# Kernel tuning notes

Hardware: AMD Instinct MI355X
Metric: run time of the kernel (lower is better)

The kernel has to match this reference:

```python
import jax, jax.numpy as jnp
import numpy as np

N, E, IN_DIM, H, D, EDGE_DIM, T = 50000, 800000, 128, 4, 32, 32, 8
NEG_SLOPE = 0.2


def setup_inputs() -> dict:
    key = jax.random.key(0)
    ks = jax.random.split(key, 12)
    s = 0.1  # xavier-ish scale
    return {
        "h": jax.random.normal(ks[0], (N, IN_DIM), jnp.float32),
        "W": jax.random.normal(ks[1], (IN_DIM, D * H), jnp.float32) * s,
        "edge_emb": jax.random.normal(ks[2], (T, EDGE_DIM), jnp.float32) * s,
        "W_r": jax.random.normal(ks[3], (T, EDGE_DIM, EDGE_DIM * H), jnp.float32) * s,
        "a_l": jax.random.normal(ks[4], (1, H, D), jnp.float32) * s,
        "a_r": jax.random.normal(ks[5], (1, H, D), jnp.float32) * s,
        "a_e": jax.random.normal(ks[6], (1, H, EDGE_DIM), jnp.float32) * s,
        "res_w": jax.random.normal(ks[7], (IN_DIM, D * H), jnp.float32) * s,
        "res_b": jnp.zeros((D * H,), jnp.float32),
        "row": jax.random.randint(ks[8], (E,), 0, N),  # src node per edge
        "col": jax.random.randint(ks[9], (E,), 0, N),  # dst node per edge
        "etype": jax.random.randint(ks[10], (E,), 0, T),
    }


def reference(h, W, edge_emb, W_r, a_l, a_r, a_e, res_w, res_b, row, col, etype):
    # node projection: [N, H, D]
    emb = (h @ W).reshape(-1, H, D)

    # TypedLinear on edge-type embeddings. Since edge features depend only on
    # etype, compute the per-type result once, then gather per edge.
    e_t = jnp.einsum('te,tef->tf', edge_emb, W_r).reshape(T, H, EDGE_DIM)
    h_e_t = (a_e * e_t).sum(-1)            # [T, H]

    h_l = (a_l * emb).sum(-1)              # [N, H]
    h_r = (a_r * emb).sum(-1)              # [N, H]
    scores = h_l[row] + h_r[col] + h_e_t[etype]          # [E, H]
    scores = jax.nn.leaky_relu(scores, NEG_SLOPE)

    # segment softmax over edges sharing the same destination node (col)
    m = jax.ops.segment_max(scores, col, num_segments=N)  # [N, H]
    ex = jnp.exp(scores - m[col])
    denom = jax.ops.segment_sum(ex, col, num_segments=N)
    alpha = ex / denom[col]                # [E, H]

    # u_mul_e + scatter-sum to destination nodes
    msg = emb[row] * alpha[:, :, None]     # [E, H, D]
    agg = jax.ops.segment_sum(msg, col, num_segments=N)   # [N, H, D]

    # original permutes to [N, D, H] before flattening (d-major layout)
    out = jnp.transpose(agg, (0, 2, 1)).reshape(-1, D * H)
    out = out + h @ res_w + res_b          # residual
    return jax.nn.elu(out)
```

## Files before the change

kernel.cpp:

```cpp
#include <hip/hip_runtime.h>
#include <math.h>

#define NH 4
#define EDIM 32
#define NEG_SLOPE 0.2f
#define BSH 5
#define CHK 32

typedef __attribute__((ext_vector_type(8))) short short8;
typedef __attribute__((ext_vector_type(4))) float f32x4;
typedef __attribute__((ext_vector_type(2))) float f32x2;

__device__ __forceinline__ unsigned short f2bf(float f) {
    unsigned int x = __builtin_bit_cast(unsigned int, f);
    unsigned int r = (x + 0x7fffu + ((x >> 16) & 1u)) >> 16;
    return (unsigned short)r;
}
__device__ __forceinline__ float bf2f(unsigned short u) {
    unsigned int x = ((unsigned int)u) << 16;
    return __builtin_bit_cast(float, x);
}

__global__ __launch_bounds__(256) void k_prep(
    const float* __restrict__ W, const float* __restrict__ Rw,
    unsigned short* __restrict__ Wt, unsigned short* __restrict__ Rwt,
    const float* __restrict__ edge_emb, const float* __restrict__ W_r,
    const float* __restrict__ a_e, float* __restrict__ h_e_t)
{
    int tid = threadIdx.x;
    if (blockIdx.x < 64) {
        int idx = blockIdx.x * 256 + tid;
        int n = idx >> 7, k = idx & 127;
        Wt[n * 128 + k]  = f2bf(W[k * 128 + n]);
        Rwt[n * 128 + k] = f2bf(Rw[k * 128 + n]);
        return;
    }
    int t = blockIdx.x - 64;
    if (tid < 128) {
        int rem = tid;
        float v = 0.f;
#pragma unroll
        for (int e = 0; e < EDIM; ++e)
            v += edge_emb[t * EDIM + e] * W_r[(size_t)(t * EDIM + e) * 128 + rem];
        v *= a_e[rem];
#pragma unroll
        for (int off = 16; off >= 1; off >>= 1)
            v += __shfl_xor(v, off);
        if ((rem & 31) == 0) h_e_t[t * NH + (rem >> 5)] = v;
    }
}

__global__ __launch_bounds__(256) void k_gemm_fill(
    const float* __restrict__ A, const unsigned short* __restrict__ Wt,
    const unsigned short* __restrict__ Rwt, const float* __restrict__ Rb,
    const float* __restrict__ a_l, const float* __restrict__ a_r,
    unsigned short* __restrict__ EmbBf, unsigned short* __restrict__ ResBf,
    float* __restrict__ h_l, float* __restrict__ h_r, int M,
    const int* __restrict__ row, const int* __restrict__ col,
    const int* __restrict__ etype, int* __restrict__ cnt,
    unsigned* __restrict__ ebuf, int E, int NB, int nFill)
{
    __shared__ char lds[32768];
    int tid = threadIdx.x;

    if ((int)blockIdx.x < nFill) {
        int* bins = (int*)lds;
        for (int i = tid; i < NB; i += 256) bins[i] = 0;
        __syncthreads();
        int fb = blockIdx.x;
        int lo = fb * 8192;
#pragma unroll 8
        for (int u = 0; u < 32; ++u) {
            int i = lo + tid + u * 256;
            if (i < E) {
                int c = col[i];
                int bk = c >> BSH;
                int slot = atomicAdd(&bins[bk], 1);
                if (slot < CHK)
                    ebuf[((size_t)bk * nFill + fb) * CHK + slot] =
                        (unsigned)row[i] | ((unsigned)etype[i] << 16)
                      | ((unsigned)(c & 31) << 24);
            }
        }
        __syncthreads();
        for (int i = tid; i < NB; i += 256) {
            int c = bins[i]; if (c > CHK) c = CHK;
            cnt[i * nFill + fb] = c;
        }
        return;
    }

    int m0 = ((int)blockIdx.x - nFill) * 64;
#pragma unroll
    for (int i = 0; i < 4; ++i) {
        int c = tid + 256 * i;
        int r = c >> 4, kc = c & 15;
        int grow = m0 + r;
        float4 v0 = make_float4(0.f, 0.f, 0.f, 0.f), v1 = v0;
        if (grow < M) {
            v0 = *(const float4*)&A[(size_t)grow * 128 + kc * 8];
            v1 = *(const float4*)&A[(size_t)grow * 128 + kc * 8 + 4];
        }
        union { unsigned short u[8]; uint4 v; } p;
        p.u[0] = f2bf(v0.x); p.u[1] = f2bf(v0.y); p.u[2] = f2bf(v0.z); p.u[3] = f2bf(v0.w);
        p.u[4] = f2bf(v1.x); p.u[5] = f2bf(v1.y); p.u[6] = f2bf(v1.z); p.u[7] = f2bf(v1.w);
        int b = (r * 256 + kc * 16) ^ ((r & 7) << 4);
        *(uint4*)&lds[b] = p.v;
    }

    int w = tid >> 6, lane = tid & 63;
    int g = lane >> 4, l15 = lane & 15;
    int lrow = w * 16 + l15;

    auto stageB = [&](const unsigned short* src) {
#pragma unroll
        for (int i = 0; i < 4; ++i) {
            int c = tid + 256 * i;
            int n2 = c >> 4, kc = c & 15;
            uint4 v = *(const uint4*)&src[n2 * 128 + kc * 8];
            int b = 16384 + ((n2 * 256 + kc * 16) ^ ((n2 & 7) << 4));
            *(uint4*)&lds[b] = v;
        }
    };
    auto computeHalf = [&](f32x4* accp, const short8* a) {
#pragma unroll
        for (int f = 0; f < 4; ++f) {
            int n2 = f * 16 + l15;
            int nsw = (n2 & 7) << 4;
#pragma unroll
            for (int s = 0; s < 4; ++s) {
                short8 b = *(const short8*)&lds[16384 + ((n2 * 256 + s * 64 + g * 16) ^ nsw)];
                accp[f] = __builtin_amdgcn_mfma_f32_16x16x32_bf16(a[s], b, accp[f], 0, 0, 0);
            }
        }
    };

    stageB(Wt);
    __syncthreads();

    short8 a[4];
#pragma unroll
    for (int s = 0; s < 4; ++s)
        a[s] = *(const short8*)&lds[(lrow * 256 + s * 64 + g * 16) ^ ((lrow & 7) << 4)];

    f32x4 acc[8];
#pragma unroll
    for (int f = 0; f < 8; ++f) acc[f] = (f32x4){0.f, 0.f, 0.f, 0.f};

    computeHalf(&acc[0], a);
    __syncthreads();
    stageB(Wt + 64 * 128);
    __syncthreads();
    computeHalf(&acc[4], a);

#pragma unroll
    for (int f = 0; f < 8; ++f) {
        int col2 = f * 16 + l15;
#pragma unroll
        for (int reg = 0; reg < 4; ++reg) {
            int grow = m0 + w * 16 + g * 4 + reg;
            if (grow < M) EmbBf[(size_t)grow * 128 + col2] = f2bf(acc[f][reg]);
        }
    }
    {
        float alv[8], arv[8];
#pragma unroll
        for (int f = 0; f < 8; ++f) {
            alv[f] = a_l[f * 16 + l15];
            arv[f] = a_r[f * 16 + l15];
        }
#pragma unroll
        for (int reg = 0; reg < 4; ++reg) {
            float4 hl4, hr4;
#pragma unroll
            for (int hh = 0; hh < 4; ++hh) {
                float pl = alv[2 * hh] * acc[2 * hh][reg] + alv[2 * hh + 1] * acc[2 * hh + 1][reg];
                float pr = arv[2 * hh] * acc[2 * hh][reg] + arv[2 * hh + 1] * acc[2 * hh + 1][reg];
#pragma unroll
                for (int off = 8; off >= 1; off >>= 1) {
                    pl += __shfl_xor(pl, off);
                    pr += __shfl_xor(pr, off);
                }
                (&hl4.x)[hh] = pl;
                (&hr4.x)[hh] = pr;
            }
            int grow = m0 + w * 16 + g * 4 + reg;
            if (l15 == 0 && grow < M) {
                *(float4*)&h_l[(size_t)grow * 4] = hl4;
                *(float4*)&h_r[(size_t)grow * 4] = hr4;
            }
        }
    }

    __syncthreads();
    stageB(Rwt);
    __syncthreads();
#pragma unroll
    for (int f = 0; f < 8; ++f) acc[f] = (f32x4){0.f, 0.f, 0.f, 0.f};
    computeHalf(&acc[0], a);
    __syncthreads();
    stageB(Rwt + 64 * 128);
    __syncthreads();
    computeHalf(&acc[4], a);

#pragma unroll
    for (int f = 0; f < 8; ++f) {
        int col2 = f * 16 + l15;
        float bias = Rb[col2];
#pragma unroll
        for (int reg = 0; reg < 4; ++reg) {
            int grow = m0 + w * 16 + g * 4 + reg;
            if (grow < M) ResBf[(size_t)grow * 128 + col2] = f2bf(acc[f][reg] + bias);
        }
    }
}

__global__ __launch_bounds__(512) void k_sort_aggregate(
    const unsigned* __restrict__ ebuf, const int* __restrict__ cnt, int nF,
    const float* __restrict__ h_l, const float* __restrict__ h_e_t,
    const float* __restrict__ h_r, const unsigned short* __restrict__ embBf,
    const unsigned short* __restrict__ resBf, float* __restrict__ out, int N)
{
    __shared__ int stage[1024];
    __shared__ int sedge[1024];
    __shared__ int chcnt[128];
    __shared__ int choff[132];
    __shared__ int cnt32[32];
    __shared__ int scn32[33];
    __shared__ char shalpha[8 * 1536];

    int b = blockIdx.x;
    int tid = threadIdx.x;
    int w = tid >> 6, lane = tid & 63;

    if (tid < 32) cnt32[tid] = 0;
    if (tid < 64) {
        int i0 = tid * 2, i1 = i0 + 1;
        int c0 = (i0 < nF) ? cnt[(size_t)b * nF + i0] : 0;
        int c1 = (i1 < nF) ? cnt[(size_t)b * nF + i1] : 0;
        chcnt[i0] = c0; chcnt[i1] = c1;
        int s = c0 + c1;
#pragma unroll
        for (int off = 1; off < 64; off <<= 1) {
            int u2 = __shfl_up(s, off);
            if (tid >= off) s += u2;
        }
        choff[i0] = s - c1 - c0;
        choff[i1] = s - c1;
        if (tid == 63) choff[128] = s;
    }
    __syncthreads();
    int m = choff[128];

#pragma unroll
    for (int itc = 0; itc < 2; ++itc) {
        int ch = itc * 64 + (tid >> 3);
        int sl = tid & 7;
        int c = chcnt[ch];
        if (sl < c) {
            int v = (int)ebuf[((size_t)b * nF + ch) * CHK + sl];
            stage[choff[ch] + sl] = v;
            atomicAdd(&cnt32[(v >> 24) & 31], 1);
        }
    }
    for (int ch = w; ch < 128; ch += 8) {
        int c = chcnt[ch];
        if (c > 8 && lane < c - 8) {
            int v = (int)ebuf[((size_t)b * nF + ch) * CHK + 8 + lane];
            stage[choff[ch] + 8 + lane] = v;
            atomicAdd(&cnt32[(v >> 24) & 31], 1);
        }
    }
    __syncthreads();

    if (tid < 32) {
        int v = cnt32[tid];
        int s = v;
#pragma unroll
        for (int off = 1; off < 32; off <<= 1) {
            int u2 = __shfl_up(s, off);
            if (tid >= off) s += u2;
        }
        scn32[tid + 1] = s;
        if (tid == 0) scn32[0] = 0;
        cnt32[tid] = s - v;
    }
    __syncthreads();
    for (int i = tid; i < m; i += 512) {
        int e = stage[i];
        int p = atomicAdd(&cnt32[(e >> 24) & 31], 1);
        sedge[p] = e & 0x00FFFFFF;
    }
    __syncthreads();

    int myh = lane >> 4;
    int l31 = lane & 31;
    int sel = lane >> 5;
    int hq = l31 >> 3;
    int loff = l31 * 8;
    char* wb = &shalpha[w * 1536];
    const char* ab2 = wb + 256 + hq * 260;
    const char* embByte = (const char*)embBf;

    for (int it = 0; it < 4; ++it) {
        int nd = it * 8 + w;
        int n = b * 32 + nd;
        if (n >= N) break;
        int st0 = scn32[nd];
        int deg = scn32[nd + 1] - st0;
        float4 hrv = *(const float4*)&h_r[(size_t)n * 4];

        if (deg <= 64) {
            bool act = lane < deg;
            float p0 = 0.f, p1 = 0.f, p2 = 0.f, p3 = 0.f;
            int roval = 0;
            if (act) {
                int pk = sedge[st0 + lane];
                roval = (pk & 0xffff) << 8;
                float4 hl = *(const float4*)&h_l[(size_t)(pk & 0xffff) * 4];
                float4 he = *(const float4*)&h_e_t[(size_t)(pk >> 16) * 4];
                float sc0 = hl.x + he.x + hrv.x; sc0 = sc0 > 0.f ? sc0 : NEG_SLOPE * sc0;
                float sc1 = hl.y + he.y + hrv.y; sc1 = sc1 > 0.f ? sc1 : NEG_SLOPE * sc1;
                float sc2 = hl.z + he.z + hrv.z; sc2 = sc2 > 0.f ? sc2 : NEG_SLOPE * sc2;
                float sc3 = hl.w + he.w + hrv.w; sc3 = sc3 > 0.f ? sc3 : NEG_SLOPE * sc3;
                p0 = __expf(sc0); p1 = __expf(sc1);
                p2 = __expf(sc2); p3 = __expf(sc3);
            }
            *(int*)(wb + lane * 4) = roval;
            *(float*)(wb + 256 + 0 * 260 + lane * 4) = p0;
            *(float*)(wb + 256 + 1 * 260 + lane * 4) = p1;
            *(float*)(wb + 256 + 2 * 260 + lane * 4) = p2;
            *(float*)(wb + 256 + 3 * 260 + lane * 4) = p3;

            float d0 = p0, d1 = p1, d2 = p2, d3 = p3;
#pragma unroll
            for (int off = 32; off >= 1; off >>= 1) {
                d0 += __shfl_xor(d0, off); d1 += __shfl_xor(d1, off);
                d2 += __shfl_xor(d2, off); d3 += __shfl_xor(d3, off);
            }
            float den = hq == 0 ? d0 : hq == 1 ? d1 : hq == 2 ? d2 : d3;
            float inv = (deg > 0) ? __builtin_amdgcn_rcpf(den) : 0.f;

            f32x4 acc4 = (f32x4){0.f, 0.f, 0.f, 0.f};
            for (int q = 0; q < deg; q += 8) {
                int ro[4]; float aq[4];
#pragma unroll
                for (int u = 0; u < 4; ++u) {
                    int qe = q + 2 * u + sel;
                    ro[u] = *(const int*)(wb + qe * 4);
                    aq[u] = *(const float*)(ab2 + qe * 4);
                }
                uint2 ev[4];
#pragma unroll
                for (int u = 0; u < 4; ++u)
                    ev[u] = *(const uint2*)(embByte + (size_t)(unsigned)(ro[u] + loff));
#pragma unroll
                for (int u = 0; u < 4; ++u) {
                    f32x4 ef;
                    ef.x = __builtin_bit_cast(float, ev[u].x << 16);
                    ef.y = __builtin_bit_cast(float, ev[u].x & 0xffff0000u);
                    ef.z = __builtin_bit_cast(float, ev[u].y << 16);
                    ef.w = __builtin_bit_cast(float, ev[u].y & 0xffff0000u);
                    acc4 = __builtin_elementwise_fma(
                        ef, (f32x4){aq[u], aq[u], aq[u], aq[u]}, acc4);
                }
            }
            acc4.x += __shfl_xor(acc4.x, 32);
            acc4.y += __shfl_xor(acc4.y, 32);
            acc4.z += __shfl_xor(acc4.z, 32);
            acc4.w += __shfl_xor(acc4.w, 32);
            float vlo = sel ? acc4.z : acc4.x;
            float vhi = sel ? acc4.w : acc4.y;

            int j0 = l31 * 4 + sel * 2;
            int h0 = j0 >> 5, dd = j0 & 31;
            size_t ob = (size_t)n * 128;
            float o0 = vlo * inv + bf2f(resBf[ob + dd * 4 + h0]);
            float o1 = vhi * inv + bf2f(resBf[ob + (dd + 1) * 4 + h0]);
            out[ob + dd * 4 + h0] = o0 > 0.f ? o0 : expm1f(o0);
            out[ob + (dd + 1) * 4 + h0] = o1 > 0.f ? o1 : expm1f(o1);
        } else {
            f32x2 acc2 = (f32x2){0.f, 0.f};
            float d0 = 0.f, d1 = 0.f, d2 = 0.f, d3 = 0.f;
            for (int base2 = 0; base2 < deg; base2 += 64) {
                int el = base2 + lane;
                if (el < deg) {
                    int pk = sedge[st0 + el];
                    float4 hl = *(const float4*)&h_l[(size_t)(pk & 0xffff) * 4];
                    float4 he = *(const float4*)&h_e_t[(size_t)(pk >> 16) * 4];
                    float sc0 = hl.x + he.x + hrv.x; sc0 = sc0 > 0.f ? sc0 : NEG_SLOPE * sc0;
                    float sc1 = hl.y + he.y + hrv.y; sc1 = sc1 > 0.f ? sc1 : NEG_SLOPE * sc1;
                    float sc2 = hl.z + he.z + hrv.z; sc2 = sc2 > 0.f ? sc2 : NEG_SLOPE * sc2;
                    float sc3 = hl.w + he.w + hrv.w; sc3 = sc3 > 0.f ? sc3 : NEG_SLOPE * sc3;
                    d0 += __expf(sc0); d1 += __expf(sc1);
                    d2 += __expf(sc2); d3 += __expf(sc3);
                }
            }
#pragma unroll
            for (int off = 32; off >= 1; off >>= 1) {
                d0 += __shfl_xor(d0, off); d1 += __shfl_xor(d1, off);
                d2 += __shfl_xor(d2, off); d3 += __shfl_xor(d3, off);
            }
            float den = myh == 0 ? d0 : myh == 1 ? d1 : myh == 2 ? d2 : d3;
            float inv = __builtin_amdgcn_rcpf(den);
            for (int base2 = 0; base2 < deg; base2 += 64) {
                int el = base2 + lane;
                float p0 = 0.f, p1 = 0.f, p2 = 0.f, p3 = 0.f;
                int r = 0;
                if (el < deg) {
                    int pk = sedge[st0 + el];
                    r = pk & 0xffff;
                    float4 hl = *(const float4*)&h_l[(size_t)r * 4];
                    float4 he = *(const float4*)&h_e_t[(size_t)(pk >> 16) * 4];
                    float sc0 = hl.x + he.x + hrv.x; sc0 = sc0 > 0.f ? sc0 : NEG_SLOPE * sc0;
                    float sc1 = hl.y + he.y + hrv.y; sc1 = sc1 > 0.f ? sc1 : NEG_SLOPE * sc1;
                    float sc2 = hl.z + he.z + hrv.z; sc2 = sc2 > 0.f ? sc2 : NEG_SLOPE * sc2;
                    float sc3 = hl.w + he.w + hrv.w; sc3 = sc3 > 0.f ? sc3 : NEG_SLOPE * sc3;
                    p0 = __expf(sc0); p1 = __expf(sc1);
                    p2 = __expf(sc2); p3 = __expf(sc3);
                }
                int cmax = (deg - base2 < 64) ? (deg - base2) : 64;
                for (int qq = 0; qq < cmax; ++qq) {
                    int rq = __shfl(r, qq);
                    float a0 = __shfl(p0, qq), a1 = __shfl(p1, qq);
                    float a2 = __shfl(p2, qq), a3 = __shfl(p3, qq);
                    float aqv = myh == 0 ? a0 : myh == 1 ? a1 : myh == 2 ? a2 : a3;
                    unsigned int ev = *(const unsigned int*)&embBf[(size_t)rq * 128 + lane * 2];
                    f32x2 ef;
                    ef.x = __builtin_bit_cast(float, ev << 16);
                    ef.y = __builtin_bit_cast(float, ev & 0xffff0000u);
                    acc2 = __builtin_elementwise_fma(ef, (f32x2){aqv, aqv}, acc2);
                }
            }
            int j0 = lane * 2;
            int h0 = j0 >> 5, dd0 = j0 & 31;
            size_t ob = (size_t)n * 128;
            float o0 = acc2.x * inv + bf2f(resBf[ob + dd0 * 4 + h0]);
            float o1 = acc2.y * inv + bf2f(resBf[ob + (dd0 + 1) * 4 + h0]);
            out[ob + dd0 * 4 + h0] = o0 > 0.f ? o0 : expm1f(o0);
            out[ob + (dd0 + 1) * 4 + h0] = o1 > 0.f ? o1 : expm1f(o1);
        }
    }
}

extern "C" void kernel_launch(void* const* d_in, const int* in_sizes, int n_in,
                              void* d_out, int out_size, void* d_ws, size_t ws_size,
                              hipStream_t stream)
{
    const float* h        = (const float*)d_in[0];
    const float* W        = (const float*)d_in[1];
    const float* edge_emb = (const float*)d_in[2];
    const float* W_r      = (const float*)d_in[3];
    const float* a_l      = (const float*)d_in[4];
    const float* a_r      = (const float*)d_in[5];
    const float* a_e      = (const float*)d_in[6];
    const float* res_w    = (const float*)d_in[7];
    const float* res_b    = (const float*)d_in[8];
    const int*   row      = (const int*)d_in[9];
    const int*   col      = (const int*)d_in[10];
    const int*   etype    = (const int*)d_in[11];
    float* out = (float*)d_out;

    int N = in_sizes[0] / 128;
    int E = in_sizes[9];
    int T = in_sizes[2] / EDIM;
    int NB = (N + 31) >> BSH;

    int nFill = (E + 8191) / 8192;
    int nGemm = (N + 63) / 64;

    char* ws = (char*)d_ws;
    size_t off = 0;
    auto alloc = [&](size_t bytes) -> char* {
        char* p = ws + off;
        off = (off + bytes + 255) & ~(size_t)255;
        return p;
    };
    unsigned short* embBf = (unsigned short*)alloc((size_t)N * 128 * 2);
    unsigned short* resBf = (unsigned short*)alloc((size_t)N * 128 * 2);
    unsigned short* Wt    = (unsigned short*)alloc((size_t)128 * 128 * 2);
    unsigned short* Rwt   = (unsigned short*)alloc((size_t)128 * 128 * 2);
    float* h_l   = (float*)alloc((size_t)N * 4 * 4);
    float* h_r   = (float*)alloc((size_t)N * 4 * 4);
    float* h_e_t = (float*)alloc((size_t)T * NH * 4);
    int* cnt     = (int*)alloc((size_t)NB * nFill * 4);
    unsigned* ebuf = (unsigned*)alloc((size_t)NB * nFill * CHK * 4);

    hipLaunchKernelGGL(k_prep, dim3(64 + T), dim3(256), 0, stream,
                       W, res_w, Wt, Rwt, edge_emb, W_r, a_e, h_e_t);
    hipLaunchKernelGGL(k_gemm_fill, dim3(nFill + nGemm), dim3(256), 0, stream,
                       h, Wt, Rwt, res_b, a_l, a_r, embBf, resBf, h_l, h_r, N,
                       row, col, etype, cnt, ebuf, E, NB, nFill);
    hipLaunchKernelGGL(k_sort_aggregate, dim3(NB), dim3(512), 0, stream,
                       ebuf, cnt, nFill, h_l, h_e_t, h_r, embBf, resBf, out, N);
}
```

Baseline: 84.25 us.

## Replace fixed-capacity edge bins with compact per-block counting sort

Result: slower. 91.61 us (+8.7%).

```diff
diff --git a/kernel.cpp b/kernel.cpp
--- a/kernel.cpp
+++ b/kernel.cpp
@@ -5,7 +5,6 @@
 #define EDIM 32
 #define NEG_SLOPE 0.2f
 #define BSH 5
-#define CHK 32
 
 typedef __attribute__((ext_vector_type(8))) short short8;
 typedef __attribute__((ext_vector_type(4))) float f32x4;
@@ -57,7 +56,7 @@
     unsigned short* __restrict__ EmbBf, unsigned short* __restrict__ ResBf,
     float* __restrict__ h_l, float* __restrict__ h_r, int M,
     const int* __restrict__ row, const int* __restrict__ col,
-    const int* __restrict__ etype, int* __restrict__ cnt,
+    const int* __restrict__ etype, unsigned* __restrict__ meta,
     unsigned* __restrict__ ebuf, int E, int NB, int nFill)
 {
     __shared__ char lds[32768];
@@ -65,27 +64,48 @@
 
     if ((int)blockIdx.x < nFill) {
         int* bins = (int*)lds;
-        for (int i = tid; i < NB; i += 256) bins[i] = 0;
+        int* wtot = bins + 2048;
+        for (int i = tid; i < 2048; i += 256) bins[i] = 0;
         __syncthreads();
         int fb = blockIdx.x;
         int lo = fb * 8192;
-#pragma unroll 8
-        for (int u = 0; u < 32; ++u) {
-            int i = lo + tid + u * 256;
-            if (i < E) {
-                int c = col[i];
-                int bk = c >> BSH;
-                int slot = atomicAdd(&bins[bk], 1);
-                if (slot < CHK)
-                    ebuf[((size_t)bk * nFill + fb) * CHK + slot] =
-                        (unsigned)row[i] | ((unsigned)etype[i] << 16)
-                      | ((unsigned)(c & 31) << 24);
-            }
-        }
+        int hi = lo + 8192 < E ? lo + 8192 : E;
+        for (int i = lo + tid; i < hi; i += 256)
+            atomicAdd(&bins[col[i] >> BSH], 1);
         __syncthreads();
-        for (int i = tid; i < NB; i += 256) {
-            int c = bins[i]; if (c > CHK) c = CHK;
-            cnt[i * nFill + fb] = c;
+        int c[8];
+        int S = 0;
+#pragma unroll
+        for (int u = 0; u < 8; ++u) { c[u] = bins[tid * 8 + u]; S += c[u]; }
+        int w_ = tid >> 6, lane_ = tid & 63;
+        int s = S;
+#pragma unroll
+        for (int off = 1; off < 64; off <<= 1) {
+            int y = __shfl_up(s, off);
+            if (lane_ >= off) s += y;
+        }
+        if (lane_ == 63) wtot[w_] = s;
+        __syncthreads();
+        int base = s - S;
+        for (int ww = 0; ww < w_; ++ww) base += wtot[ww];
+        __syncthreads();
+#pragma unroll
+        for (int u = 0; u < 8; ++u) {
+            int bk = tid * 8 + u;
+            bins[bk] = base;
+            if (bk < NB) {
+                int cc = c[u] < 255 ? c[u] : 255;
+                meta[(size_t)fb * NB + bk] = (unsigned)((base << 8) | cc);
+            }
+            base += c[u];
+        }
+        __syncthreads();
+        for (int i = lo + tid; i < hi; i += 256) {
+            int cc = col[i];
+            int bk = cc >> BSH;
+            int p = atomicAdd(&bins[bk], 1);
+            ebuf[lo + p] = (unsigned)row[i] | ((unsigned)etype[i] << 16)
+                         | ((unsigned)(cc & 31) << 24);
         }
         return;
     }
@@ -216,7 +236,8 @@
 }
 
 __global__ __launch_bounds__(512) void k_sort_aggregate(
-    const unsigned* __restrict__ ebuf, const int* __restrict__ cnt, int nF,
+    const unsigned* __restrict__ ebuf, const unsigned* __restrict__ meta,
+    int nF, int NB,
     const float* __restrict__ h_l, const float* __restrict__ h_e_t,
     const float* __restrict__ h_r, const unsigned short* __restrict__ embBf,
     const unsigned short* __restrict__ resBf, float* __restrict__ out, int N)
@@ -224,6 +245,7 @@
     __shared__ int stage[1024];
     __shared__ int sedge[1024];
     __shared__ int chcnt[128];
+    __shared__ int chbase[128];
     __shared__ int choff[132];
     __shared__ int cnt32[32];
     __shared__ int scn32[33];
@@ -236,9 +258,11 @@
     if (tid < 32) cnt32[tid] = 0;
     if (tid < 64) {
         int i0 = tid * 2, i1 = i0 + 1;
-        int c0 = (i0 < nF) ? cnt[(size_t)b * nF + i0] : 0;
-        int c1 = (i1 < nF) ? cnt[(size_t)b * nF + i1] : 0;
+        unsigned m0v = (i0 < nF) ? meta[(size_t)i0 * NB + b] : 0u;
+        unsigned m1v = (i1 < nF) ? meta[(size_t)i1 * NB + b] : 0u;
+        int c0 = (int)(m0v & 255u), c1 = (int)(m1v & 255u);
         chcnt[i0] = c0; chcnt[i1] = c1;
+        chbase[i0] = (int)(m0v >> 8); chbase[i1] = (int)(m1v >> 8);
         int s = c0 + c1;
 #pragma unroll
         for (int off = 1; off < 64; off <<= 1) {
@@ -258,7 +282,7 @@
         int sl = tid & 7;
         int c = chcnt[ch];
         if (sl < c) {
-            int v = (int)ebuf[((size_t)b * nF + ch) * CHK + sl];
+            int v = (int)ebuf[ch * 8192 + chbase[ch] + sl];
             stage[choff[ch] + sl] = v;
             atomicAdd(&cnt32[(v >> 24) & 31], 1);
         }
@@ -266,7 +290,7 @@
     for (int ch = w; ch < 128; ch += 8) {
         int c = chcnt[ch];
         if (c > 8 && lane < c - 8) {
-            int v = (int)ebuf[((size_t)b * nF + ch) * CHK + 8 + lane];
+            int v = (int)ebuf[ch * 8192 + chbase[ch] + 8 + lane];
             stage[choff[ch] + 8 + lane] = v;
             atomicAdd(&cnt32[(v >> 24) & 31], 1);
         }
@@ -483,14 +507,14 @@
     float* h_l   = (float*)alloc((size_t)N * 4 * 4);
     float* h_r   = (float*)alloc((size_t)N * 4 * 4);
     float* h_e_t = (float*)alloc((size_t)T * NH * 4);
-    int* cnt     = (int*)alloc((size_t)NB * nFill * 4);
-    unsigned* ebuf = (unsigned*)alloc((size_t)NB * nFill * CHK * 4);
+    unsigned* meta = (unsigned*)alloc((size_t)nFill * NB * 4);
+    unsigned* ebuf = (unsigned*)alloc((size_t)nFill * 8192 * 4);
 
     hipLaunchKernelGGL(k_prep, dim3(64 + T), dim3(256), 0, stream,
                        W, res_w, Wt, Rwt, edge_emb, W_r, a_e, h_e_t);
     hipLaunchKernelGGL(k_gemm_fill, dim3(nFill + nGemm), dim3(256), 0, stream,
                        h, Wt, Rwt, res_b, a_l, a_r, embBf, resBf, h_l, h_r, N,
-                       row, col, etype, cnt, ebuf, E, NB, nFill);
+                       row, col, etype, meta, ebuf, E, NB, nFill);
     hipLaunchKernelGGL(k_sort_aggregate, dim3(NB), dim3(512), 0, stream,
-                       ebuf, cnt, nFill, h_l, h_e_t, h_r, embBf, resBf, out, N);
+                       ebuf, meta, nFill, NB, h_l, h_e_t, h_r, embBf, resBf, out, N);
 }
```
